# Optimization experiments

Hardware: AMD Instinct MI355X
Metric: run time of the kernel (lower is better)

Reference implementation:

```python
import jax, jax.numpy as jnp
import numpy as np

AH, AW, TD = 7, 7, 4
SPATIAL_SCALE = 0.0625
TEMP_SCALE = 1.0


def setup_inputs() -> dict:
    key = jax.random.key(0)
    ks = jax.random.split(key, 8)
    N, C, T, H, W = 2, 256, 16, 64, 64
    R = 1024
    features = jax.random.normal(ks[0], (N, C, T, H, W), dtype=jnp.float32)
    img = W / SPATIAL_SCALE  # 1024 px original image
    b = jax.random.randint(ks[1], (R,), 0, N).astype(jnp.float32)
    x1 = jax.random.uniform(ks[2], (R,), minval=0.0, maxval=img * 0.7)
    y1 = jax.random.uniform(ks[3], (R,), minval=0.0, maxval=img * 0.7)
    x2 = x1 + jax.random.uniform(ks[4], (R,), minval=32.0, maxval=img * 0.3)
    y2 = y1 + jax.random.uniform(ks[5], (R,), minval=32.0, maxval=img * 0.3)
    t1 = jax.random.uniform(ks[6], (R,), minval=0.0, maxval=(T - 1) * 0.5)
    t2 = t1 + jax.random.uniform(ks[7], (R,), minval=1.0, maxval=(T - 1) * 0.5)
    rois = jnp.stack([b, x1, y1, t1, x2, y2, t2], axis=1)  # [R,7]
    return {"features": features, "rois": rois}


def _axis_samples(start, end, n, size):
    # legacy roi_align: n grid points spanning the roi, bin = extent/(n-1)
    bin_sz = jnp.maximum(end - start, 0.0) / (n - 1)
    c = start[:, None] + bin_sz[:, None] * jnp.arange(n, dtype=start.dtype)  # [R,n]
    lo = jnp.clip(jnp.floor(c), 0, size - 2).astype(jnp.int32)
    return lo, c - lo, (c >= 0) & (c < size)


def _roi_align_avg(features, rois):
    N, C, T, H, W = features.shape
    Tg, Hg, Wg = TD + 1, AH + 1, AW + 1  # sample on a +1 grid, then avg-pool back
    b = rois[:, 0].astype(jnp.int32)
    t0, ft, vt = _axis_samples(rois[:, 3] * TEMP_SCALE, rois[:, 6] * TEMP_SCALE, Tg, T)
    h0, fh, vh = _axis_samples(rois[:, 2] * SPATIAL_SCALE, rois[:, 5] * SPATIAL_SCALE, Hg, H)
    w0, fw, vw = _axis_samples(rois[:, 1] * SPATIAL_SCALE, rois[:, 4] * SPATIAL_SCALE, Wg, W)
    fm = jnp.transpose(features, (0, 2, 3, 4, 1))  # [N,T,H,W,C] channel-last gather
    b4 = b[:, None, None, None]
    R = rois.shape[0]
    out = jnp.zeros((R, Tg, Hg, Wg, C), dtype=features.dtype)
    for dt in (0, 1):  # 8-corner trilinear interpolation
        wt = ft if dt else (1.0 - ft)
        for dh in (0, 1):
            wh = fh if dh else (1.0 - fh)
            for dw in (0, 1):
                ww = fw if dw else (1.0 - fw)
                corner = fm[b4,
                            (t0 + dt)[:, :, None, None],
                            (h0 + dh)[:, None, :, None],
                            (w0 + dw)[:, None, None, :]]  # [R,Tg,Hg,Wg,C]
                w8 = wt[:, :, None, None] * wh[:, None, :, None] * ww[:, None, None, :]
                out = out + w8[..., None] * corner
    valid = vt[:, :, None, None] & vh[:, None, :, None] & vw[:, None, None, :]
    out = out * valid[..., None].astype(out.dtype)  # samples outside feature map -> 0

    def pool_pairs(a, axis):
        # adaptive_avg_pool from K+1 -> K == kernel-2 stride-1 average
        n = a.shape[axis]
        return 0.5 * (jax.lax.slice_in_dim(a, 0, n - 1, axis=axis)
                      + jax.lax.slice_in_dim(a, 1, n, axis=axis))

    out = pool_pairs(pool_pairs(pool_pairs(out, 1), 2), 3)  # [R,TD,AH,AW,C]
    return jnp.transpose(out, (0, 4, 1, 2, 3))  # [R,C,TD,AH,AW]


def reference(features, rois):
    return _roi_align_avg(features, rois)
```

## Files before the change

kernel.cpp:

```cpp
#include <hip/hip_runtime.h>

#define C_CH 256
#define T_SZ 16
#define H_SZ 64
#define W_SZ 64
#define TGN 5
#define CH 8
#define HWs (H_SZ * W_SZ)
#define CSTR (T_SZ * HWs)
#define NOUT 196
#define KMAX 10

__device__ __forceinline__ float2 ld2(const float* p) {
    float2 v;
    __builtin_memcpy(&v, p, sizeof(float2));
    return v;
}

__global__ __launch_bounds__(256, 8) void roialign3d_kernel(
    const float* __restrict__ features,
    const float* __restrict__ rois,
    float* __restrict__ out)
{
    const int bid   = blockIdx.x;
    const int sr    = bid >> 13;
    const int rem   = bid & 8191;
    const int r     = rem >> 3;
    const int chunk = (sr << 3) | (rem & 7);
    const int c0    = chunk * CH;

    const int tid  = threadIdx.x;
    const int lane = tid & 63;
    const int wid  = __builtin_amdgcn_readfirstlane(tid >> 6);
    const int hg   = lane >> 3;
    const int wg   = lane & 7;

    __shared__ __align__(16) float sB[KMAX][4];
    __shared__ int sU0, sK;

    const float* roi = rois + r * 7;
    const int   b   = __builtin_amdgcn_readfirstlane((int)roi[0]);
    const float rx1 = roi[1], ry1 = roi[2];
    const float rx2 = roi[4], ry2 = roi[5];

    if (tid < KMAX) {
        const float rt1 = roi[3], rt2 = roi[6];
        const float tbin = fmaxf(rt2 - rt1, 0.0f) * 0.25f;
        int t0a[TGN]; float tw0a[TGN], tw1a[TGN];
        #pragma unroll
        for (int i = 0; i < TGN; ++i) {
            float c  = rt1 + tbin * (float)i;
            float lo = fminf(fmaxf(floorf(c), 0.0f), 14.0f);
            float f  = c - lo;
            float v  = (c >= 0.0f && c < 16.0f) ? 0.125f : 0.0f;
            t0a[i]  = (int)lo;
            tw0a[i] = v * (1.0f - f);
            tw1a[i] = v * f;
        }
        const int u0 = t0a[0];
        const int s0 = u0 + tid;
        float av[TGN];
        #pragma unroll
        for (int i = 0; i < TGN; ++i)
            av[i] = (t0a[i] == s0 ? tw0a[i] : 0.0f)
                  + (t0a[i] + 1 == s0 ? tw1a[i] : 0.0f);
        sB[tid][0] = av[0] + av[1];
        sB[tid][1] = av[1] + av[2];
        sB[tid][2] = av[2] + av[3];
        sB[tid][3] = av[3] + av[4];
        if (tid == 0) { sU0 = u0; sK = t0a[TGN - 1] + 2 - u0; }
    }

    const float hs = ry1 * 0.0625f, he = ry2 * 0.0625f;
    const float hbin = fmaxf(he - hs, 0.0f) * (1.0f / 7.0f);
    const float hc  = hs + hbin * (float)hg;
    const float hlo = fminf(fmaxf(floorf(hc), 0.0f), 62.0f);
    const float hf  = hc - hlo;
    const float hv  = (hc >= 0.0f && hc < 64.0f) ? 1.0f : 0.0f;
    const int   h0  = (int)hlo;
    const float hw0 = hv * (1.0f - hf), hw1 = hv * hf;

    const float wss = rx1 * 0.0625f, wee = rx2 * 0.0625f;
    const float wbin = fmaxf(wee - wss, 0.0f) * (1.0f / 7.0f);
    const float wc  = wss + wbin * (float)wg;
    const float wlo = fminf(fmaxf(floorf(wc), 0.0f), 62.0f);
    const float wf  = wc - wlo;
    const float wv  = (wc >= 0.0f && wc < 64.0f) ? 1.0f : 0.0f;
    const int   w0  = (int)wlo;
    const float ww0 = wv * (1.0f - wf), ww1 = wv * wf;

    const float w00 = hw0 * ww0, w01 = hw0 * ww1;
    const float w10 = hw1 * ww0, w11 = hw1 * ww1;
    const int hw_off = h0 * W_SZ + w0;

    __syncthreads();
    const int u0   = __builtin_amdgcn_readfirstlane(sU0);
    const int kcnt = __builtin_amdgcn_readfirstlane(sK);

    const bool active = (hg < 7) && (wg < 7);
    const int  s_hw   = hg * 7 + wg;

    const float* fcA = features
        + ((size_t)b * C_CH + (size_t)(c0 + wid * 2)) * CSTR
        + (size_t)u0 * HWs + hw_off;
    const float* fcB = fcA + CSTR;

    float oA[4] = {0.f, 0.f, 0.f, 0.f};
    float oB[4] = {0.f, 0.f, 0.f, 0.f};

    #pragma unroll
    for (int u = 0; u < KMAX; ++u) {
        if (u < 2 || u < kcnt) {
            const float4 bb = *(const float4*)sB[u];
            const float* pA = fcA + u * HWs;
            const float* pB = fcB + u * HWs;
            float2 rA0 = ld2(pA);
            float2 rA1 = ld2(pA + W_SZ);
            float2 rB0 = ld2(pB);
            float2 rB1 = ld2(pB + W_SZ);

            const float bilA = rA0.x * w00 + rA0.y * w01 + rA1.x * w10 + rA1.y * w11;
            const float bilB = rB0.x * w00 + rB0.y * w01 + rB1.x * w10 + rB1.y * w11;

            oA[0] += bb.x * bilA; oA[1] += bb.y * bilA;
            oA[2] += bb.z * bilA; oA[3] += bb.w * bilA;
            oB[0] += bb.x * bilB; oB[1] += bb.y * bilB;
            oB[2] += bb.z * bilB; oB[3] += bb.w * bilB;
        }
    }

    float* ob = out + ((size_t)r * C_CH + (size_t)(c0 + wid * 2)) * NOUT;
    #pragma unroll
    for (int td = 0; td < 4; ++td) {
        float o = oA[td];
        o += __shfl_down(o, 1);
        o += __shfl_down(o, 8);
        if (active) __builtin_nontemporal_store(o, &ob[td * 49 + s_hw]);
    }
    ob += NOUT;
    #pragma unroll
    for (int td = 0; td < 4; ++td) {
        float o = oB[td];
        o += __shfl_down(o, 1);
        o += __shfl_down(o, 8);
        if (active) __builtin_nontemporal_store(o, &ob[td * 49 + s_hw]);
    }
}

extern "C" void kernel_launch(void* const* d_in, const int* in_sizes, int n_in,
                              void* d_out, int out_size, void* d_ws, size_t ws_size,
                              hipStream_t stream) {
    const float* features = (const float*)d_in[0];
    const float* rois     = (const float*)d_in[1];
    float* out            = (float*)d_out;

    int R = in_sizes[1] / 7;
    int nblocks = R * (C_CH / CH);
    hipLaunchKernelGGL(roialign3d_kernel, dim3(nblocks), dim3(256), 0, stream,
                       features, rois, out);
}
```

Measured before the change: 133.5 us.

## Stage ROI feature window into per-wave LDS with coalesced float4 loads and prefetch

Each wave now loads the ROI's row window for each temporal slice as coalesced float4 segments into a padded per-wave LDS tile. The bilinear corners are then read from LDS instead of from scattered per-lane float2 global gathers. The next slice is prefetched into registers while the current one is computed. A 16- or 32-wide window variant is picked at runtime from the ROI width. LDS use goes up and launch bounds drop to 6 blocks, so occupancy may fall.

After: 164.8 us. 23.5% more time.

```diff
diff --git a/kernel.cpp b/kernel.cpp
--- a/kernel.cpp
+++ b/kernel.cpp
@@ -11,13 +11,118 @@
 #define NOUT 196
 #define KMAX 10
 
-__device__ __forceinline__ float2 ld2(const float* p) {
-    float2 v;
-    __builtin_memcpy(&v, p, sizeof(float2));
-    return v;
-}
-
-__global__ __launch_bounds__(256, 8) void roialign3d_kernel(
+__device__ __forceinline__ float4 ld4(const float* p) {
+    return *(const float4*)p;
+}
+
+__device__ __forceinline__ int h0_of(float hs, float hbin, int g) {
+    return (int)fminf(fmaxf(floorf(hs + hbin * (float)g), 0.0f), 62.0f);
+}
+
+template<int WPAD>
+__device__ __forceinline__ void sample_loop(
+    const float* fc,
+    float* sbuf,
+    const float (*sBt)[4],
+    int kcnt, int wbase,
+    float hs, float hbin,
+    int lane, int hg, int w0,
+    float w00, float w01, float w10, float w11,
+    float oA[4], float oB[4])
+{
+    constexpr int STR  = WPAD + 1;
+    constexpr int TILE = 16 * STR;
+    constexpr int NL   = (WPAD == 16) ? 2 : 4;
+
+    int goffA, goffB = 0, woff;
+    if constexpr (WPAD == 16) {
+        const int dh   = (lane >> 2) & 1;
+        const int unit = lane & 3;
+        const int hh   = h0_of(hs, hbin, lane >> 3);
+        goffA = (hh + dh) * W_SZ + wbase + unit * 4;
+        woff  = (lane >> 2) * STR + unit * 4;
+    } else {
+        const int dh   = (lane >> 3) & 1;
+        const int unit = lane & 7;
+        const int hA   = h0_of(hs, hbin, lane >> 4);
+        const int hB   = h0_of(hs, hbin, 4 + (lane >> 4));
+        goffA = (hA + dh) * W_SZ + wbase + unit * 4;
+        goffB = (hB + dh) * W_SZ + wbase + unit * 4;
+        woff  = (lane >> 3) * STR + unit * 4;
+    }
+    const int w0l = w0 - wbase;
+    const int ro  = hg * 2 * STR + w0l;
+
+    float4 g[NL];
+    if constexpr (WPAD == 16) {
+        g[0] = ld4(fc + goffA);
+        g[1] = ld4(fc + CSTR + goffA);
+        #pragma unroll
+        for (int i = 0; i < 2; ++i) {
+            float* d = sbuf + i * TILE + woff;
+            d[0] = g[i].x; d[1] = g[i].y; d[2] = g[i].z; d[3] = g[i].w;
+        }
+    } else {
+        g[0] = ld4(fc + goffA);
+        g[1] = ld4(fc + goffB);
+        g[2] = ld4(fc + CSTR + goffA);
+        g[3] = ld4(fc + CSTR + goffB);
+        #pragma unroll
+        for (int i = 0; i < 4; ++i) {
+            float* d = sbuf + (i >> 1) * TILE + (i & 1) * 8 * STR + woff;
+            d[0] = g[i].x; d[1] = g[i].y; d[2] = g[i].z; d[3] = g[i].w;
+        }
+    }
+
+    #pragma unroll
+    for (int u = 0; u < KMAX; ++u) {
+        if (u < kcnt) {
+            const bool more = (u + 1 < kcnt);
+            float4 gn[NL];
+            if (more) {
+                const float* fu = fc + (u + 1) * HWs;
+                if constexpr (WPAD == 16) {
+                    gn[0] = ld4(fu + goffA);
+                    gn[1] = ld4(fu + CSTR + goffA);
+                } else {
+                    gn[0] = ld4(fu + goffA);
+                    gn[1] = ld4(fu + goffB);
+                    gn[2] = ld4(fu + CSTR + goffA);
+                    gn[3] = ld4(fu + CSTR + goffB);
+                }
+            }
+            const float4 bb = *(const float4*)sBt[u];
+            const float a00 = sbuf[ro],              a01 = sbuf[ro + 1];
+            const float a10 = sbuf[ro + STR],        a11 = sbuf[ro + STR + 1];
+            const float c00 = sbuf[ro + TILE],       c01 = sbuf[ro + TILE + 1];
+            const float c10 = sbuf[ro + TILE + STR], c11 = sbuf[ro + TILE + STR + 1];
+            const float bilA = a00 * w00 + a01 * w01 + a10 * w10 + a11 * w11;
+            const float bilB = c00 * w00 + c01 * w01 + c10 * w10 + c11 * w11;
+            oA[0] += bb.x * bilA; oA[1] += bb.y * bilA;
+            oA[2] += bb.z * bilA; oA[3] += bb.w * bilA;
+            oB[0] += bb.x * bilB; oB[1] += bb.y * bilB;
+            oB[2] += bb.z * bilB; oB[3] += bb.w * bilB;
+
+            if (more) {
+                if constexpr (WPAD == 16) {
+                    #pragma unroll
+                    for (int i = 0; i < 2; ++i) {
+                        float* d = sbuf + i * TILE + woff;
+                        d[0] = gn[i].x; d[1] = gn[i].y; d[2] = gn[i].z; d[3] = gn[i].w;
+                    }
+                } else {
+                    #pragma unroll
+                    for (int i = 0; i < 4; ++i) {
+                        float* d = sbuf + (i >> 1) * TILE + (i & 1) * 8 * STR + woff;
+                        d[0] = gn[i].x; d[1] = gn[i].y; d[2] = gn[i].z; d[3] = gn[i].w;
+                    }
+                }
+            }
+        }
+    }
+}
+
+__global__ __launch_bounds__(256, 6) void roialign3d_kernel(
     const float* __restrict__ features,
     const float* __restrict__ rois,
     float* __restrict__ out)
@@ -37,6 +142,7 @@
 
     __shared__ __align__(16) float sB[KMAX][4];
     __shared__ int sU0, sK;
+    __shared__ float stg[4][2 * 16 * 33];
 
     const float* roi = rois + r * 7;
     const int   b   = __builtin_amdgcn_readfirstlane((int)roi[0]);
@@ -91,44 +197,33 @@
 
     const float w00 = hw0 * ww0, w01 = hw0 * ww1;
     const float w10 = hw1 * ww0, w11 = hw1 * ww1;
-    const int hw_off = h0 * W_SZ + w0;
 
     __syncthreads();
     const int u0   = __builtin_amdgcn_readfirstlane(sU0);
     const int kcnt = __builtin_amdgcn_readfirstlane(sK);
 
+    const int w0min = (int)fminf(fmaxf(floorf(wss), 0.0f), 62.0f);
+    const int w0max = (int)fminf(fmaxf(floorf(wss + 7.0f * wbin), 0.0f), 62.0f);
+    const int wb16  = min(w0min & ~3, H_SZ - 16);
+    const int wb32  = min(w0min & ~3, H_SZ - 32);
+    const bool use16 = (w0max - wb16) <= 14;
+
+    const float* fc = features
+        + ((size_t)b * C_CH + (size_t)(c0 + wid * 2)) * CSTR
+        + (size_t)u0 * HWs;
+
+    float oA[4] = {0.f, 0.f, 0.f, 0.f};
+    float oB[4] = {0.f, 0.f, 0.f, 0.f};
+
+    if (use16)
+        sample_loop<16>(fc, stg[wid], sB, kcnt, wb16, hs, hbin,
+                        lane, hg, w0, w00, w01, w10, w11, oA, oB);
+    else
+        sample_loop<32>(fc, stg[wid], sB, kcnt, wb32, hs, hbin,
+                        lane, hg, w0, w00, w01, w10, w11, oA, oB);
+
     const bool active = (hg < 7) && (wg < 7);
     const int  s_hw   = hg * 7 + wg;
-
-    const float* fcA = features
-        + ((size_t)b * C_CH + (size_t)(c0 + wid * 2)) * CSTR
-        + (size_t)u0 * HWs + hw_off;
-    const float* fcB = fcA + CSTR;
-
-    float oA[4] = {0.f, 0.f, 0.f, 0.f};
-    float oB[4] = {0.f, 0.f, 0.f, 0.f};
-
-    #pragma unroll
-    for (int u = 0; u < KMAX; ++u) {
-        if (u < 2 || u < kcnt) {
-            const float4 bb = *(const float4*)sB[u];
-            const float* pA = fcA + u * HWs;
-            const float* pB = fcB + u * HWs;
-            float2 rA0 = ld2(pA);
-            float2 rA1 = ld2(pA + W_SZ);
-            float2 rB0 = ld2(pB);
-            float2 rB1 = ld2(pB + W_SZ);
-
-            const float bilA = rA0.x * w00 + rA0.y * w01 + rA1.x * w10 + rA1.y * w11;
-            const float bilB = rB0.x * w00 + rB0.y * w01 + rB1.x * w10 + rB1.y * w11;
-
-            oA[0] += bb.x * bilA; oA[1] += bb.y * bilA;
-            oA[2] += bb.z * bilA; oA[3] += bb.w * bilA;
-            oB[0] += bb.x * bilB; oB[1] += bb.y * bilB;
-            oB[2] += bb.z * bilB; oB[3] += bb.w * bilB;
-        }
-    }
-
     float* ob = out + ((size_t)r * C_CH + (size_t)(c0 + wid * 2)) * NOUT;
     #pragma unroll
     for (int td = 0; td < 4; ++td) {
```
